# Kernel optimization log

Hardware: AMD Instinct MI355X
Metric: run time of the kernel (lower is better)

Reference implementation:

```python
import jax, jax.numpy as jnp
import numpy as np

D = 256  # hardcoded Dense units in the original layer

def setup_inputs() -> dict:
    key = jax.random.key(0)
    ks = jax.random.split(key, 7)
    B, S, F = 8, 2048, 256
    x = jax.random.normal(ks[0], (B, S, F), dtype=jnp.float32)
    # Dense layers (kernel + bias), glorot-ish scale
    scale = 1.0 / np.sqrt(F)
    Wq = jax.random.normal(ks[1], (F, D), dtype=jnp.float32) * scale
    Wk = jax.random.normal(ks[2], (F, D), dtype=jnp.float32) * scale
    Wv = jax.random.normal(ks[3], (F, D), dtype=jnp.float32) * scale
    bq = jax.random.normal(ks[4], (D,), dtype=jnp.float32) * 0.01
    bk = jax.random.normal(ks[5], (D,), dtype=jnp.float32) * 0.01
    bv = jax.random.normal(ks[6], (D,), dtype=jnp.float32) * 0.01
    return {"x": x, "Wq": Wq, "bq": bq, "Wk": Wk, "bk": bk, "Wv": Wv, "bv": bv}

def reference(x, Wq, bq, Wk, bk, Wv, bv):
    # Q/K/V projections: Dense(256) == x @ W + b
    Q = jnp.einsum('bsf,fd->bsd', x, Wq) + bq
    K = jnp.einsum('bsf,fd->bsd', x, Wk) + bk
    V = jnp.einsum('bsf,fd->bsd', x, Wv) + bv
    scores = jnp.einsum('bqd,bkd->bqk', Q, K) / jnp.sqrt(jnp.float32(D))
    attn = jax.nn.softmax(scores, axis=-1)
    return jnp.einsum('bqk,bkd->bqd', attn, V)
```

## Files before the change

kernel.cpp:

```cpp
#include <hip/hip_runtime.h>

typedef __bf16 bf16;
typedef __bf16 bf16x4v __attribute__((ext_vector_type(4)));
typedef __bf16 bf16x8 __attribute__((ext_vector_type(8)));
typedef float f32x4 __attribute__((ext_vector_type(4)));
typedef short s16x4 __attribute__((ext_vector_type(4)));

#define MFMA_X32(A, B, C) __builtin_amdgcn_mfma_f32_16x16x32_bf16(A, B, C, 0, 0, 0)

static __device__ __forceinline__ float fast_exp2(float x) {
  float r;
  asm volatile("v_exp_f32 %0, %1\n\ts_nop 0" : "=v"(r) : "v"(x));
  return r;
}

static __device__ __forceinline__ void gll16(const void* g, void* l) {
  __builtin_amdgcn_global_load_lds(
      (const __attribute__((address_space(1))) void*)g,
      (__attribute__((address_space(3))) void*)l, 16, 0, 0);
}

#define WT_OFF 0
#define Q_OFF 393216
#define K_OFF 8781824
#define V_OFF 17170432

__global__ __launch_bounds__(256) void prep_wt(const float* __restrict__ Wq,
                                               const float* __restrict__ Wk,
                                               const float* __restrict__ Wv,
                                               bf16* __restrict__ Wt) {
  const int idx = blockIdx.x * 256 + threadIdx.x;
  const int p = idx >> 16;
  const int rem = idx & 65535;
  const int k = rem >> 8, n = rem & 255;
  const float* W = (p == 0) ? Wq : ((p == 1) ? Wk : Wv);
  Wt[p * 65536 + n * 256 + k] = (bf16)W[rem];
}

__global__ __launch_bounds__(256, 3) void proj_qkv(const float* __restrict__ x,
                                                   const float* __restrict__ bq,
                                                   const float* __restrict__ bk,
                                                   const float* __restrict__ bv,
                                                   char* __restrict__ ws0) {
  __shared__ __align__(16) char smem[40960];
  const bf16* Wt = (const bf16*)(ws0 + WT_OFF);
  bf16* Qo = (bf16*)(ws0 + Q_OFF);
  bf16* Ko = (bf16*)(ws0 + K_OFF);
  bf16* Vc = (bf16*)(ws0 + V_OFF);
  const int t = threadIdx.x;
  const int lane = t & 63, w = t >> 6, l16 = lane & 15, quad = lane >> 4;
  const int fam = blockIdx.x % 6;
  const int rgroup = blockIdx.x / 6;
  const int p = fam >> 1, ch = fam & 1;
  const float* bias = (p == 0) ? bq : ((p == 1) ? bk : bv);
  const float sc = (p == 0) ? 0.09016844005556021f : 1.0f;

  const int nl = w * 32 + l16;
  bf16x8 bfr[2][8];
#pragma unroll
  for (int nt = 0; nt < 2; ++nt)
#pragma unroll
    for (int kt = 0; kt < 8; ++kt)
      bfr[nt][kt] = *(const bf16x8*)&Wt[p * 65536 + (ch * 128 + nl + nt * 16) * 256 +
                                        kt * 32 + quad * 8];
  float bias2[2];
#pragma unroll
  for (int nt = 0; nt < 2; ++nt) bias2[nt] = bias[ch * 128 + nl + nt * 16];

  const int row0 = rgroup * 128;
  char* outL = smem + 32768;

  float4 xr[4][2];
#define STAGE_LOAD(tile)                                                        \
  {                                                                             \
    const float* xp = x + (row0 + (tile) * 32) * 256;                           \
    _Pragma("unroll") for (int i = 0; i < 4; ++i) {                             \
      const int u2 = i * 256 + t, row = u2 >> 5, col8 = (u2 & 31) * 8;          \
      xr[i][0] = *(const float4*)&xp[row * 256 + col8];                         \
      xr[i][1] = *(const float4*)&xp[row * 256 + col8 + 4];                     \
    }                                                                           \
  }
#define STAGE_WRITE(buf)                                                        \
  {                                                                             \
    _Pragma("unroll") for (int i = 0; i < 4; ++i) {                             \
      const int u2 = i * 256 + t, row = u2 >> 5, col8 = (u2 & 31) * 8;          \
      const float* f0 = (const float*)&xr[i][0];                                \
      const float* f1 = (const float*)&xr[i][1];                                \
      bf16x8 h;                                                                 \
      _Pragma("unroll") for (int j = 0; j < 4; ++j) {                           \
        h[j] = (bf16)f0[j];                                                     \
        h[4 + j] = (bf16)f1[j];                                                 \
      }                                                                         \
      *(bf16x8*)&smem[(buf) * 16384 + row * 512 +                               \
                      ((col8 * 2) ^ ((row & 7) << 4))] = h;                     \
    }                                                                           \
  }

  STAGE_LOAD(0);
  STAGE_WRITE(0);
  __syncthreads();

  int cur = 0;
  for (int tt = 0; tt < 4; ++tt) {
    if (tt < 3) STAGE_LOAD(tt + 1);

    f32x4 acc[2][2];
#pragma unroll
    for (int rs = 0; rs < 2; ++rs)
#pragma unroll
      for (int nt = 0; nt < 2; ++nt) acc[rs][nt] = f32x4{0.f, 0.f, 0.f, 0.f};
    const char* xb = smem + cur * 16384;
#pragma unroll
    for (int rs = 0; rs < 2; ++rs) {
      const int row = rs * 16 + l16;
#pragma unroll
      for (int kt = 0; kt < 8; ++kt) {
        const bf16x8 a = *(const bf16x8*)(xb + row * 512 +
                                          ((kt * 64 + quad * 16) ^ ((l16 & 7) << 4)));
        acc[rs][0] = MFMA_X32(a, bfr[0][kt], acc[rs][0]);
        acc[rs][1] = MFMA_X32(a, bfr[1][kt], acc[rs][1]);
      }
    }
    __syncthreads();

#pragma unroll
    for (int rs = 0; rs < 2; ++rs)
#pragma unroll
      for (int nt = 0; nt < 2; ++nt)
#pragma unroll
        for (int r = 0; r < 4; ++r) {
          const int sl = rs * 16 + quad * 4 + r;
          const int nn = nl + nt * 16;
          const bf16 hv = (bf16)((acc[rs][nt][r] + bias2[nt]) * sc);
          int pos;
          if (p == 0)
            pos = sl * 128 + nn;
          else if (p == 1)
            pos = (sl >> 4) * 2048 + (nn >> 5) * 512 + ((nn >> 3) & 3) * 128 +
                  (sl & 15) * 8 + (nn & 7);
          else
            pos = (nn >> 4) * 512 + ((sl >> 2) & 3) * 128 + (nn & 15) * 8 +
                  (sl >> 4) * 4 + (sl & 3);
          *(bf16*)(outL + pos * 2) = hv;
        }
    if (tt < 3) STAGE_WRITE(cur ^ 1);
    __syncthreads();

    const int rowg = row0 + tt * 32;
    if (p == 0) {
      const int row = t >> 3, cb = (t & 7) * 32;
      const float4 v0 = *(const float4*)(outL + row * 256 + cb);
      const float4 v1 = *(const float4*)(outL + row * 256 + cb + 16);
      char* dst = (char*)Qo + (rowg + row) * 512 + ch * 256 + cb;
      *(float4*)dst = v0;
      *(float4*)(dst + 16) = v1;
    } else if (p == 1) {
      const int b2 = rowg >> 11, s0 = rowg & 2047;
      char* dst = (char*)Ko + b2 * 1048576 + ((s0 >> 4) + (t >> 7)) * 8192 +
                  ch * 4096 + (t & 127) * 32;
      const float4 v0 = *(const float4*)(outL + t * 32);
      const float4 v1 = *(const float4*)(outL + t * 32 + 16);
      *(float4*)dst = v0;
      *(float4*)(dst + 16) = v1;
    } else {
      const int b2 = rowg >> 11, s0 = rowg & 2047;
      char* dst = (char*)Vc + b2 * 1048576 + (s0 >> 5) * 16384 + ch * 8192 + t * 32;
      const float4 v0 = *(const float4*)(outL + t * 32);
      const float4 v1 = *(const float4*)(outL + t * 32 + 16);
      *(float4*)dst = v0;
      *(float4*)(dst + 16) = v1;
    }
    cur ^= 1;
  }
#undef STAGE_LOAD
#undef STAGE_WRITE
}

#define SLOT_SZ 16640

__global__ __launch_bounds__(512, 2) void flash_attn(const char* __restrict__ ws0,
                                                     float* __restrict__ out) {
  __shared__ __align__(1024) char smem[135168];
  const bf16* Qp = (const bf16*)(ws0 + Q_OFF);
  const int t = threadIdx.x;
  const int lane = t & 63, w = t >> 6;
  const int l16 = lane & 15, quad = lane >> 4;
  const int qs = w & 1, kq = w >> 1;
  const int b = blockIdx.x & 7;
  const int qt = blockIdx.x >> 3;
  const int qrow0 = b * 2048 + qt * 64 + qs * 32;

  bf16x8 qf[2][8];
#pragma unroll
  for (int qsub = 0; qsub < 2; ++qsub)
#pragma unroll
    for (int kt = 0; kt < 8; ++kt)
      qf[qsub][kt] =
          *(const bf16x8*)&Qp[(qrow0 + qsub * 16 + l16) * 256 + kt * 32 + quad * 8];

  f32x4 o[2][16];
#pragma unroll
  for (int qsub = 0; qsub < 2; ++qsub)
#pragma unroll
    for (int dt = 0; dt < 16; ++dt) o[qsub][dt] = f32x4{0.f, 0.f, 0.f, 0.f};
  float m_[2] = {-1e30f, -1e30f}, l_[2] = {0.f, 0.f};

  unsigned goffK[4], loffK[4];
#pragma unroll
  for (int i = 0; i < 4; ++i) {
    const int u = w * 4 + i;
    const int kq2 = u >> 3, e = u & 7;
    goffK[i] = (unsigned)K_OFF + b * 1048576u + kq2 * 262144u + e * 1024u + lane * 16u;
    loffK[i] = kq2 * 8192u + e * 1024u;
  }
  unsigned goffV[8], loffV[8];
#pragma unroll
  for (int i = 0; i < 8; ++i) {
    const int u = w * 8 + i;
    const int kqv = u >> 4, e = u & 15;
    goffV[i] = (unsigned)V_OFF + b * 1048576u + kqv * 262144u + e * 1024u + lane * 16u;
    loffV[i] = 65536u + kqv * 16384u + e * 1024u;
  }

#define STAGE_K(S)                                                             \
  {                                                                            \
    _Pragma("unroll") for (int i = 0; i < 4; ++i)                              \
        gll16(ws0 + goffK[i] + (unsigned)(S) * 8192u,                          \
              smem + (unsigned)(((S) & 1) * 32768) + loffK[i]);                \
  }
#define STAGE_V(P)                                                             \
  {                                                                            \
    _Pragma("unroll") for (int i = 0; i < 8; ++i)                              \
        gll16(ws0 + goffV[i] + (unsigned)(P) * 16384u, smem + loffV[i]);       \
  }
#define QK_STEP(CURK, KC)                                                      \
  {                                                                            \
    const char* kb = smem + (CURK) + kq * 8192 + lane * 16;                    \
    __builtin_amdgcn_s_setprio(1);                                             \
    _Pragma("unroll") for (int kt = 0; kt < 8; ++kt) {                         \
      const bf16x8 kf = *(const bf16x8*)(kb + kt * 1024);                      \
      sfr[0][KC] = MFMA_X32(kf, qf[0][kt], sfr[0][KC]);                        \
      sfr[1][KC] = MFMA_X32(kf, qf[1][kt], sfr[1][KC]);                        \
    }                                                                          \
    __builtin_amdgcn_s_setprio(0);                                             \
  }

  STAGE_K(0);

  for (int p = 0; p < 16; ++p) {
    f32x4 sfr[2][2];
#pragma unroll
    for (int qsub = 0; qsub < 2; ++qsub)
#pragma unroll
      for (int kc = 0; kc < 2; ++kc) sfr[qsub][kc] = f32x4{0.f, 0.f, 0.f, 0.f};

    __syncthreads();
    STAGE_K(2 * p + 1);
    STAGE_V(p);
    QK_STEP((unsigned)((2 * p) & 1) * 32768u, 0);

    __syncthreads();
    if (p < 15) STAGE_K(2 * p + 2);
    QK_STEP((unsigned)((2 * p + 1) & 1) * 32768u, 1);

    bf16x8 pa[2];
#pragma unroll
    for (int qsub = 0; qsub < 2; ++qsub) {
      const f32x4 sA = sfr[qsub][0], sB = sfr[qsub][1];
      const float cml = fmaxf(fmaxf(fmaxf(sA[0], sA[1]), fmaxf(sA[2], sA[3])),
                              fmaxf(fmaxf(sB[0], sB[1]), fmaxf(sB[2], sB[3])));
      const float mold = m_[qsub];
      if (__builtin_expect(__any(cml > mold + 6.0f), 0)) {
        float cm = fmaxf(cml, __shfl_xor(cml, 16));
        cm = fmaxf(cm, __shfl_xor(cm, 32));
        const float Mnew = fmaxf(mold, cm);
        const float al = fast_exp2(mold - Mnew);
        m_[qsub] = Mnew;
        l_[qsub] *= al;
        float ar[4];
#pragma unroll
        for (int r = 0; r < 4; ++r)
          ar[r] = __shfl(al, (quad << 4) + (quad << 2) + r);
#pragma unroll
        for (int dt = 0; dt < 16; ++dt)
#pragma unroll
          for (int r = 0; r < 4; ++r) o[qsub][dt][r] *= ar[r];
      }
      const float Mref = m_[qsub];
      float ps = 0.f;
#pragma unroll
      for (int r = 0; r < 4; ++r) {
        const bf16 p0 = (bf16)fast_exp2(sA[r] - Mref);
        const bf16 p1 = (bf16)fast_exp2(sB[r] - Mref);
        pa[qsub][r] = p0;
        pa[qsub][4 + r] = p1;
        ps += (float)p0 + (float)p1;
      }
      l_[qsub] += ps;
    }

    const char* vb = smem + 65536 + kq * 16384 + lane * 16;
    __builtin_amdgcn_s_setprio(1);
#pragma unroll
    for (int dt = 0; dt < 16; ++dt) {
      const bf16x8 vf = *(const bf16x8*)(vb + dt * 1024);
      o[0][dt] = MFMA_X32(pa[0], vf, o[0][dt]);
      o[1][dt] = MFMA_X32(pa[1], vf, o[1][dt]);
    }
    __builtin_amdgcn_s_setprio(0);
  }
#undef STAGE_K
#undef STAGE_V
#undef QK_STEP

#pragma unroll
  for (int qsub = 0; qsub < 2; ++qsub) {
    l_[qsub] += __shfl_xor(l_[qsub], 16);
    l_[qsub] += __shfl_xor(l_[qsub], 32);
  }

  float* mlf = (float*)(smem + 133120);
  if (quad == 0) {
#pragma unroll
    for (int qsub = 0; qsub < 2; ++qsub) {
      const int base = ((kq * 2 + qs) * 2 + qsub) * 32;
      mlf[base + l16] = m_[qsub];
      mlf[base + 16 + l16] = l_[qsub];
    }
  }
  __syncthreads();
#pragma unroll
  for (int qsub = 0; qsub < 2; ++qsub) {
    float M = -1e30f, mk[4], lk[4];
#pragma unroll
    for (int k2 = 0; k2 < 4; ++k2) {
      const int base = ((k2 * 2 + qs) * 2 + qsub) * 32;
      mk[k2] = mlf[base + l16];
      lk[k2] = mlf[base + 16 + l16];
      M = fmaxf(M, mk[k2]);
    }
    float L = 0.f;
#pragma unroll
    for (int k2 = 0; k2 < 4; ++k2) L += lk[k2] * fast_exp2(mk[k2] - M);
    const float sg = fast_exp2(m_[qsub] - M) / L;
    float sr[4];
#pragma unroll
    for (int r = 0; r < 4; ++r) sr[r] = __shfl(sg, (quad << 4) + (quad << 2) + r);
#pragma unroll
    for (int dt = 0; dt < 16; ++dt)
#pragma unroll
      for (int r = 0; r < 4; ++r) o[qsub][dt][r] *= sr[r];
  }
  if (kq >= 2) {
#pragma unroll
    for (int qsub = 0; qsub < 2; ++qsub) {
      float* sb = (float*)(smem + ((kq - 2) * 4 + qs * 2 + qsub) * SLOT_SZ);
#pragma unroll
      for (int dt = 0; dt < 16; ++dt)
#pragma unroll
        for (int r = 0; r < 4; ++r)
          sb[(quad * 4 + r) * 260 + dt * 16 + l16] = o[qsub][dt][r];
    }
  }
  __syncthreads();
  if (kq < 2) {
#pragma unroll
    for (int qsub = 0; qsub < 2; ++qsub) {
      const float* sb = (const float*)(smem + (kq * 4 + qs * 2 + qsub) * SLOT_SZ);
#pragma unroll
      for (int dt = 0; dt < 16; ++dt)
#pragma unroll
        for (int r = 0; r < 4; ++r)
          o[qsub][dt][r] += sb[(quad * 4 + r) * 260 + dt * 16 + l16];
    }
  }
  __syncthreads();
  if (kq == 1) {
#pragma unroll
    for (int qsub = 0; qsub < 2; ++qsub) {
      float* sb = (float*)(smem + (qs * 2 + qsub) * SLOT_SZ);
#pragma unroll
      for (int dt = 0; dt < 16; ++dt)
#pragma unroll
        for (int r = 0; r < 4; ++r)
          sb[(quad * 4 + r) * 260 + dt * 16 + l16] = o[qsub][dt][r];
    }
  }
  __syncthreads();
  if (kq == 0) {
#pragma unroll
    for (int qsub = 0; qsub < 2; ++qsub) {
      const float* sb = (const float*)(smem + (qs * 2 + qsub) * SLOT_SZ);
#pragma unroll
      for (int dt = 0; dt < 16; ++dt)
#pragma unroll
        for (int r = 0; r < 4; ++r) {
          const float v = o[qsub][dt][r] + sb[(quad * 4 + r) * 260 + dt * 16 + l16];
          out[(qrow0 + qsub * 16 + quad * 4 + r) * 256 + dt * 16 + l16] = v;
        }
    }
  }
}

extern "C" void kernel_launch(void* const* d_in, const int* in_sizes, int n_in,
                              void* d_out, int out_size, void* d_ws,
                              size_t ws_size, hipStream_t stream) {
  const float* x = (const float*)d_in[0];
  const float* Wq = (const float*)d_in[1];
  const float* bq = (const float*)d_in[2];
  const float* Wk = (const float*)d_in[3];
  const float* bk = (const float*)d_in[4];
  const float* Wv = (const float*)d_in[5];
  const float* bv = (const float*)d_in[6];
  float* out = (float*)d_out;
  char* ws = (char*)d_ws;

  prep_wt<<<768, 256, 0, stream>>>(Wq, Wk, Wv, (bf16*)(ws + WT_OFF));
  proj_qkv<<<768, 256, 0, stream>>>(x, bq, bk, bv, ws);
  flash_attn<<<256, 512, 0, stream>>>(ws, out);
}
```

Measured before the change: 158.5 us.

## Split V staging into halves with double-buffered first half and split QK accumulators

```diff
diff --git a/kernel.cpp b/kernel.cpp
--- a/kernel.cpp
+++ b/kernel.cpp
@@ -180,7 +180,7 @@
 
 __global__ __launch_bounds__(512, 2) void flash_attn(const char* __restrict__ ws0,
                                                      float* __restrict__ out) {
-  __shared__ __align__(1024) char smem[135168];
+  __shared__ __align__(1024) char smem[163840];
   const bf16* Qp = (const bf16*)(ws0 + Q_OFF);
   const int t = threadIdx.x;
   const int lane = t & 63, w = t >> 6;
@@ -213,13 +213,13 @@
     goffK[i] = (unsigned)K_OFF + b * 1048576u + kq2 * 262144u + e * 1024u + lane * 16u;
     loffK[i] = kq2 * 8192u + e * 1024u;
   }
-  unsigned goffV[8], loffV[8];
-#pragma unroll
-  for (int i = 0; i < 8; ++i) {
-    const int u = w * 8 + i;
-    const int kqv = u >> 4, e = u & 15;
+  unsigned goffV[4], loffV[4];
+#pragma unroll
+  for (int i = 0; i < 4; ++i) {
+    const int u = w * 4 + i;
+    const int kqv = u >> 3, e = u & 7;
     goffV[i] = (unsigned)V_OFF + b * 1048576u + kqv * 262144u + e * 1024u + lane * 16u;
-    loffV[i] = 65536u + kqv * 16384u + e * 1024u;
+    loffV[i] = kqv * 8192u + e * 1024u;
   }
 
 #define STAGE_K(S)                                                             \
@@ -228,24 +228,40 @@
         gll16(ws0 + goffK[i] + (unsigned)(S) * 8192u,                          \
               smem + (unsigned)(((S) & 1) * 32768) + loffK[i]);                \
   }
-#define STAGE_V(P)                                                             \
+#define STAGE_V_H0(P)                                                          \
   {                                                                            \
-    _Pragma("unroll") for (int i = 0; i < 8; ++i)                              \
-        gll16(ws0 + goffV[i] + (unsigned)(P) * 16384u, smem + loffV[i]);       \
+    _Pragma("unroll") for (int i = 0; i < 4; ++i)                              \
+        gll16(ws0 + goffV[i] + (unsigned)(P) * 16384u,                         \
+              smem + 65536u + (unsigned)(((P) & 1) * 32768) + loffV[i]);       \
+  }
+#define STAGE_V_H1(P)                                                          \
+  {                                                                            \
+    _Pragma("unroll") for (int i = 0; i < 4; ++i)                              \
+        gll16(ws0 + goffV[i] + (unsigned)(P) * 16384u + 8192u,                 \
+              smem + 131072u + loffV[i]);                                      \
   }
 #define QK_STEP(CURK, KC)                                                      \
   {                                                                            \
     const char* kb = smem + (CURK) + kq * 8192 + lane * 16;                    \
+    f32x4 a0 = f32x4{0.f, 0.f, 0.f, 0.f}, a1 = a0;                             \
     __builtin_amdgcn_s_setprio(1);                                             \
-    _Pragma("unroll") for (int kt = 0; kt < 8; ++kt) {                         \
+    _Pragma("unroll") for (int kt = 0; kt < 4; ++kt) {                         \
+      const bf16x8 kf = *(const bf16x8*)(kb + kt * 1024);                      \
+      a0 = MFMA_X32(kf, qf[0][kt], a0);                                        \
+      a1 = MFMA_X32(kf, qf[1][kt], a1);                                        \
+    }                                                                          \
+    _Pragma("unroll") for (int kt = 4; kt < 8; ++kt) {                         \
       const bf16x8 kf = *(const bf16x8*)(kb + kt * 1024);                      \
       sfr[0][KC] = MFMA_X32(kf, qf[0][kt], sfr[0][KC]);                        \
       sfr[1][KC] = MFMA_X32(kf, qf[1][kt], sfr[1][KC]);                        \
     }                                                                          \
     __builtin_amdgcn_s_setprio(0);                                             \
+    sfr[0][KC] += a0;                                                          \
+    sfr[1][KC] += a1;                                                          \
   }
 
   STAGE_K(0);
+  STAGE_V_H0(0);
 
   for (int p = 0; p < 16; ++p) {
     f32x4 sfr[2][2];
@@ -256,11 +272,14 @@
 
     __syncthreads();
     STAGE_K(2 * p + 1);
-    STAGE_V(p);
+    STAGE_V_H1(p);
     QK_STEP((unsigned)((2 * p) & 1) * 32768u, 0);
 
     __syncthreads();
-    if (p < 15) STAGE_K(2 * p + 2);
+    if (p < 15) {
+      STAGE_K(2 * p + 2);
+      STAGE_V_H0(p + 1);
+    }
     QK_STEP((unsigned)((2 * p + 1) & 1) * 32768u, 1);
 
     bf16x8 pa[2];
@@ -299,18 +318,27 @@
       l_[qsub] += ps;
     }
 
-    const char* vb = smem + 65536 + kq * 16384 + lane * 16;
+    const char* vb0 = smem + 65536u + (unsigned)((p & 1) * 32768) + kq * 8192 +
+                      lane * 16;
+    const char* vb1 = smem + 131072u + kq * 8192 + lane * 16;
     __builtin_amdgcn_s_setprio(1);
 #pragma unroll
-    for (int dt = 0; dt < 16; ++dt) {
-      const bf16x8 vf = *(const bf16x8*)(vb + dt * 1024);
+    for (int dt = 0; dt < 8; ++dt) {
+      const bf16x8 vf = *(const bf16x8*)(vb0 + dt * 1024);
       o[0][dt] = MFMA_X32(pa[0], vf, o[0][dt]);
       o[1][dt] = MFMA_X32(pa[1], vf, o[1][dt]);
     }
+#pragma unroll
+    for (int dt = 8; dt < 16; ++dt) {
+      const bf16x8 vf = *(const bf16x8*)(vb1 + (dt - 8) * 1024);
+      o[0][dt] = MFMA_X32(pa[0], vf, o[0][dt]);
+      o[1][dt] = MFMA_X32(pa[1], vf, o[1][dt]);
+    }
     __builtin_amdgcn_s_setprio(0);
   }
 #undef STAGE_K
-#undef STAGE_V
+#undef STAGE_V_H0
+#undef STAGE_V_H1
 #undef QK_STEP
 
 #pragma unroll
@@ -318,6 +346,8 @@
     l_[qsub] += __shfl_xor(l_[qsub], 16);
     l_[qsub] += __shfl_xor(l_[qsub], 32);
   }
+
+  __syncthreads();
 
   float* mlf = (float*)(smem + 133120);
   if (quad == 0) {
```

After: 160.3 us. No clear change (+1.1%).
